# Kernel optimization log

Measured on AMD Instinct MI355X. Metric: run time of the kernel, lower is better.

The kernel has to match this reference:

```python
import jax, jax.numpy as jnp
import numpy as np

B, N, K = 2, 8192, 16          # batch, points, ED_nsample
SA_C, DG_C = 128, 1024         # SA_conv_out, DG_conv_out
CAT_C = SA_C + SA_C // 4 + 4   # 164 channels into head


def _conv1(W, b, x):
    # 1x1 Conv1d: W [out,in], x [B,in,N]
    return jnp.einsum('oc,bcn->bon', W, x) + b[None, :, None]


def _bn_relu(x, g, be):
    # BatchNorm1d (training-mode batch stats) + ReLU, x [B,C,N]
    m = x.mean(axis=(0, 2), keepdims=True)
    v = x.var(axis=(0, 2), keepdims=True)
    return jax.nn.relu((x - m) * jax.lax.rsqrt(v + 1e-5) * g[None, :, None] + be[None, :, None])


def setup_inputs() -> dict:
    key = jax.random.key(0)
    ks = jax.random.split(key, 32)
    w = lambda k, s: jax.random.normal(k, s, jnp.float32) * 0.05
    p = {}
    p['pointcloud'] = jax.random.normal(ks[0], (B, N, 3), jnp.float32)
    p['h1'] = jax.random.normal(ks[1], (B, SA_C, N), jnp.float32)
    p['h2'] = jax.random.normal(ks[2], (B, DG_C, N), jnp.float32)
    p['numpoints'] = N
    # DG head convs 1024->256->64->32
    p['DG_w1'], p['DG_b1'] = w(ks[3], (256, DG_C)), jnp.zeros(256, jnp.float32)
    p['DG_g1'], p['DG_be1'] = jnp.ones(256, jnp.float32), jnp.zeros(256, jnp.float32)
    p['DG_w2'], p['DG_b2'] = w(ks[4], (64, 256)), jnp.zeros(64, jnp.float32)
    p['DG_g2'], p['DG_be2'] = jnp.ones(64, jnp.float32), jnp.zeros(64, jnp.float32)
    p['DG_w3'], p['DG_b3'] = w(ks[5], (SA_C // 4, 64)), jnp.zeros(SA_C // 4, jnp.float32)
    p['DG_g3'], p['DG_be3'] = jnp.ones(SA_C // 4, jnp.float32), jnp.zeros(SA_C // 4, jnp.float32)
    # ED MLP 3->4->4
    p['ED_w1'], p['ED_b1'] = w(ks[6], (3, 4)), jnp.zeros(4, jnp.float32)
    p['ED_w2'], p['ED_b2'] = w(ks[7], (4, 4)), jnp.zeros(4, jnp.float32)
    # head convs 164->512->256->128
    p['C_w1'], p['C_b1'] = w(ks[8], (512, CAT_C)), jnp.zeros(512, jnp.float32)
    p['C_g1'], p['C_be1'] = jnp.ones(512, jnp.float32), jnp.zeros(512, jnp.float32)
    p['C_w2'], p['C_b2'] = w(ks[9], (256, 512)), jnp.zeros(256, jnp.float32)
    p['C_g2'], p['C_be2'] = jnp.ones(256, jnp.float32), jnp.zeros(256, jnp.float32)
    p['C_w3'], p['C_b3'] = w(ks[10], (128, 256)), jnp.zeros(128, jnp.float32)
    p['C_g3'], p['C_be3'] = jnp.ones(128, jnp.float32), jnp.zeros(128, jnp.float32)
    return p


def reference(pointcloud, h1, h2, numpoints,
              DG_w1, DG_b1, DG_g1, DG_be1, DG_w2, DG_b2, DG_g2, DG_be2,
              DG_w3, DG_b3, DG_g3, DG_be3,
              ED_w1, ED_b1, ED_w2, ED_b2,
              C_w1, C_b1, C_g1, C_be1, C_w2, C_b2, C_g2, C_be2,
              C_w3, C_b3, C_g3, C_be3):
    xyz = pointcloud[..., :3]
    # DG branch head
    h2p = _bn_relu(_conv1(DG_w1, DG_b1, h2), DG_g1, DG_be1)
    h2p = _bn_relu(_conv1(DG_w2, DG_b2, h2p), DG_g2, DG_be2)
    h2p = _bn_relu(_conv1(DG_w3, DG_b3, h2p), DG_g3, DG_be3)
    # ED branch: brute-force knn on squared distances
    sq = jnp.sum(xyz * xyz, axis=-1)                               # [B,N]
    d = sq[:, :, None] + sq[:, None, :] - 2.0 * jnp.einsum('bnd,bmd->bnm', xyz, xyz)
    _, idx = jax.lax.top_k(-d, K)                                  # [B,N,K]
    nbr = jax.vmap(lambda pts, i: pts[i])(xyz, idx)                # [B,N,K,3]
    c = nbr - nbr.mean(axis=2, keepdims=True)
    cov = jnp.einsum('bnkd,bnke->bnde', c, c) / K                  # [B,N,3,3]
    ev = jnp.linalg.eigvalsh(cov)                                  # [B,N,3] ascending
    h3 = jax.nn.relu(ev @ ED_w1 + ED_b1) @ ED_w2 + ED_b2           # [B,N,4]
    # fuse and head
    z = jnp.concatenate([h1, h2p, jnp.transpose(h3, (0, 2, 1))], axis=1)
    z = _bn_relu(_conv1(C_w1, C_b1, z), C_g1, C_be1)
    z = _bn_relu(_conv1(C_w2, C_b2, z), C_g2, C_be2)
    z = _bn_relu(_conv1(C_w3, C_b3, z), C_g3, C_be3)
    return xyz, z
```

## Files before the change

### kernel.cpp

```cpp
#include <hip/hip_runtime.h>

#define NPTS 8192
#define BATCH 2

typedef __attribute__((ext_vector_type(8))) __bf16 bf16x8;
typedef __attribute__((ext_vector_type(4))) float f32x4;
typedef unsigned int u32;

__device__ inline unsigned short f2bf(float x) {
    unsigned u = __float_as_uint(x);
    u += 0x7fffu + ((u >> 16) & 1u);
    return (unsigned short)(u >> 16);
}
__device__ inline unsigned pack32(float d, unsigned idx) {
    unsigned u = __float_as_uint(d);
    u ^= ((unsigned)((int)u >> 31)) | 0x80000000u;
    return (u & 0xFFFFE000u) | idx;
}
__device__ inline unsigned bitonic64u(unsigned key, int lane) {
#pragma unroll
    for (int k = 2; k <= 64; k <<= 1) {
#pragma unroll
        for (int j = k >> 1; j > 0; j >>= 1) {
            unsigned o = __shfl_xor(key, j, 64);
            bool tmin = (((lane & k) == 0) == ((lane & j) == 0));
            key = ((o < key) == tmin) ? o : key;
        }
    }
    return key;
}
__device__ inline void ins16(unsigned& key, unsigned c, int lane) {
    unsigned prev = __shfl_up(key, 1, 64);
    if (lane == 0) prev = 0u;
    unsigned mx = prev > c ? prev : c;
    key = mx < key ? mx : key;
}
__device__ inline float distf(float4 q, float4 p) {
    return fmaf(-2.f, fmaf(q.z, p.z, fmaf(q.y, p.y, q.x * p.x)), q.w + p.w);
}

__global__ __launch_bounds__(256) void prep_presplit(
    const float* __restrict__ pc, float* __restrict__ oxyz, float4* __restrict__ pq,
    const float* __restrict__ W0, const float* __restrict__ W1,
    const float* __restrict__ W2, const float* __restrict__ W3,
    const float* __restrict__ W4, const float* __restrict__ W5,
    unsigned short* __restrict__ wsp) {
    int bx = blockIdx.x, tid = threadIdx.x;
    if (bx < 64) {
        int t = bx * 256 + tid;
        float x = pc[t * 3 + 0], y = pc[t * 3 + 1], z = pc[t * 3 + 2];
        oxyz[t * 3 + 0] = x; oxyz[t * 3 + 1] = y; oxyz[t * 3 + 2] = z;
        pq[t] = make_float4(x, y, z, fmaf(z, z, fmaf(y, y, x * x)));
        return;
    }
    int pb = bx - 64;
    const float* W; int O, C, OP; size_t off; int base;
    if (pb < 1024)      { W = W0; O = 256; C = 1024; OP = 256; off = 0;       base = 0; }
    else if (pb < 1152) { W = W1; O =  64; C =  256; OP = 128; off = 524288;  base = 1024; }
    else if (pb < 1184) { W = W2; O =  32; C =   64; OP = 128; off = 589824;  base = 1152; }
    else if (pb < 1568) { W = W3; O = 512; C =  164; OP = 512; off = 606208;  base = 1184; }
    else if (pb < 2080) { W = W4; O = 256; C =  512; OP = 256; off = 802816;  base = 1568; }
    else                { W = W5; O = 128; C =  256; OP = 128; off = 1064960; base = 2080; }
    unsigned short* dst = wsp + off;
    int t = (pb - base) * 256 + tid;
    int kk = t & 31;
    int o = (t >> 5) % OP;
    int kt = t / (OP * 32);
    int c = kt * 32 + kk;
    float x = (o < O && c < C) ? W[o * C + c] : 0.f;
    unsigned short hb = f2bf(x);
    float hf = __uint_as_float((unsigned)hb << 16);
    unsigned short lb = f2bf(x - hf);
    int s = kk >> 3, pos = kk & 7;
    int sst = s ^ ((o >> 1) & 3);
    dst[((size_t)(kt * 2) * OP + o) * 32 + sst * 8 + pos] = hb;
    dst[((size_t)(kt * 2 + 1) * OP + o) * 32 + sst * 8 + pos] = lb;
}

template <int MODE>
__global__ __launch_bounds__(256, 4) void mfma_gemm(
    const unsigned short* __restrict__ Wsp, const float* __restrict__ bias,
    const float* __restrict__ X, float* __restrict__ out,
    int O, int C, int OP, int nK,
    const float2* __restrict__ stats,
    const float* __restrict__ h1, const float* __restrict__ h3,
    const float2* __restrict__ stats3,
    float2* __restrict__ partout) {
    const int N = NPTS;
    int tid = threadIdx.x;
    int lane = tid & 63, w = tid >> 6;
    int wm = w >> 1, wn = w & 1;
    int b = blockIdx.z, n0 = blockIdx.x * 64, o0 = blockIdx.y * 64;
    int nblk = blockIdx.x;
    int n = n0 + lane;

    __shared__ __align__(16) unsigned char lds[18432];
    __shared__ float ps1[2][64], ps2[2][64];
    unsigned char* WHp = lds;
    unsigned char* WLp = lds + 4096;
    unsigned char* XHp = lds + 8192;
    unsigned char* XLp = lds + 13312;

    f32x4 acc[2][2];
#pragma unroll
    for (int i = 0; i < 2; ++i)
#pragma unroll
        for (int j = 0; j < 2; ++j) acc[i][j] = (f32x4){0.f, 0.f, 0.f, 0.f};

    float xcur[8], xnxt[8];
    auto loadx = [&](int kt, float (&dst)[8]) {
#pragma unroll
        for (int i = 0; i < 8; ++i) {
            int c = kt * 32 + w * 8 + i;
            float x = 0.f;
            if (MODE == 0 || MODE == 1) {
                if (c < C) x = X[((size_t)(b * C + c)) * N + n];
            } else {
                if (c < 128)       x = h1[((size_t)(b * 128 + c)) * N + n];
                else if (c < 160)  x = X[((size_t)(b * 32 + (c - 128))) * N + n];
                else if (c < 164)  x = h3[((size_t)(b * 4 + (c - 160))) * N + n];
            }
            dst[i] = x;
        }
    };

    loadx(0, xcur);
    for (int kt = 0; kt < nK; ++kt) {
        int c0 = kt * 32;
#pragma unroll
        for (int comp = 0; comp < 2; ++comp) {
            const unsigned short* gb = Wsp + ((size_t)(kt * 2 + comp) * OP + o0) * 32;
            unsigned char* lb = comp ? WLp : WHp;
            __builtin_amdgcn_global_load_lds(
                (const __attribute__((address_space(1))) u32*)(gb + w * 512 + lane * 8),
                (__attribute__((address_space(3))) u32*)(lb + w * 1024),
                16, 0, 0);
        }
        {
            union { bf16x8 s; unsigned short u[8]; } hh, ll;
#pragma unroll
            for (int i = 0; i < 8; ++i) {
                int c = c0 + w * 8 + i;
                float x = xcur[i];
                if (MODE == 1) {
                    if (c < C) {
                        float2 st = stats[c];
                        x = fmaxf(fmaf(x, st.x, st.y), 0.f);
                    }
                } else if (MODE == 2) {
                    if (c >= 128 && c < 160) {
                        float2 st = stats3[c - 128];
                        x = fmaxf(fmaf(x, st.x, st.y), 0.f);
                    }
                }
                unsigned short hb = f2bf(x);
                float hf = __uint_as_float((unsigned)hb << 16);
                unsigned short lb = f2bf(x - hf);
                hh.u[i] = hb; ll.u[i] = lb;
            }
            *(bf16x8*)(XHp + lane * 80 + w * 16) = hh.s;
            *(bf16x8*)(XLp + lane * 80 + w * 16) = ll.s;
        }
        if (kt + 1 < nK) loadx(kt + 1, xnxt);
        __syncthreads();
        {
            int koff = (lane >> 4) * 16;
            bf16x8 bh[2], bl[2];
#pragma unroll
            for (int ni = 0; ni < 2; ++ni) {
                int rb = wn * 32 + ni * 16 + (lane & 15);
                bh[ni] = *(const bf16x8*)(XHp + rb * 80 + koff);
                bl[ni] = *(const bf16x8*)(XLp + rb * 80 + koff);
            }
#pragma unroll
            for (int mi = 0; mi < 2; ++mi) {
                int ra = wm * 32 + mi * 16 + (lane & 15);
                int sw = koff ^ ((((unsigned)ra >> 1) & 3) * 16);
                bf16x8 ah = *(const bf16x8*)(WHp + ra * 64 + sw);
                bf16x8 al = *(const bf16x8*)(WLp + ra * 64 + sw);
#pragma unroll
                for (int ni = 0; ni < 2; ++ni) {
                    acc[mi][ni] = __builtin_amdgcn_mfma_f32_16x16x32_bf16(ah, bh[ni], acc[mi][ni], 0, 0, 0);
                    acc[mi][ni] = __builtin_amdgcn_mfma_f32_16x16x32_bf16(ah, bl[ni], acc[mi][ni], 0, 0, 0);
                    acc[mi][ni] = __builtin_amdgcn_mfma_f32_16x16x32_bf16(al, bh[ni], acc[mi][ni], 0, 0, 0);
                }
            }
        }
        __syncthreads();
        if (kt + 1 < nK) {
#pragma unroll
            for (int i = 0; i < 8; ++i) xcur[i] = xnxt[i];
        }
    }
    int col = lane & 15, rq = lane >> 4;
#pragma unroll
    for (int mi = 0; mi < 2; ++mi) {
#pragma unroll
        for (int j = 0; j < 4; ++j) {
            int oloc = wm * 32 + mi * 16 + rq * 4 + j;
            int o = o0 + oloc;
            float s1 = 0.f, s2 = 0.f;
            if (o < O) {
                float bs = bias[o];
                float v0 = acc[mi][0][j] + bs;
                float v1 = acc[mi][1][j] + bs;
                float* po = out + ((size_t)(b * O + o)) * N + n0 + wn * 32 + col;
                po[0] = v0; po[16] = v1;
                s1 = v0 + v1;
                s2 = fmaf(v0, v0, v1 * v1);
            }
#pragma unroll
            for (int mm = 1; mm < 16; mm <<= 1) {
                s1 += __shfl_xor(s1, mm, 64);
                s2 += __shfl_xor(s2, mm, 64);
            }
            if (col == 0) { ps1[wn][oloc] = s1; ps2[wn][oloc] = s2; }
        }
    }
    __syncthreads();
    if (tid < 64) {
        int o = o0 + tid;
        if (o < O)
            partout[(size_t)o * 256 + b * 128 + nblk] =
                make_float2(ps1[0][tid] + ps1[1][tid], ps2[0][tid] + ps2[1][tid]);
    }
}

__global__ __launch_bounds__(256) void finalize_kernel(const float2* __restrict__ part,
                                                       const float* __restrict__ g,
                                                       const float* __restrict__ be,
                                                       float2* __restrict__ st) {
    int c = blockIdx.x;
    int tid = threadIdx.x;
    __shared__ float r1[256], r2[256];
    float2 v = part[(size_t)c * 256 + tid];
    r1[tid] = v.x; r2[tid] = v.y;
    __syncthreads();
    for (int off = 128; off > 0; off >>= 1) {
        if (tid < off) { r1[tid] += r1[tid + off]; r2[tid] += r2[tid + off]; }
        __syncthreads();
    }
    if (tid == 0) {
        const float inv = 1.f / (BATCH * NPTS);
        float m = r1[0] * inv;
        float var = r2[0] * inv - m * m;
        float sc = g[c] * rsqrtf(var + 1e-5f);
        st[c] = make_float2(sc, be[c] - m * sc);
    }
}

__global__ __launch_bounds__(256) void stats_final_kernel(
    const float2* __restrict__ part, const float* __restrict__ g,
    const float* __restrict__ be, const float* __restrict__ X,
    float* __restrict__ outz) {
    const int N = NPTS;
    const int C = 128;
    int c = blockIdx.x;
    int tid = threadIdx.x;
    __shared__ float r1[256], r2[256];
    __shared__ float2 stv;
    float2 v = part[(size_t)c * 256 + tid];
    r1[tid] = v.x; r2[tid] = v.y;
    __syncthreads();
    for (int off = 128; off > 0; off >>= 1) {
        if (tid < off) { r1[tid] += r1[tid + off]; r2[tid] += r2[tid + off]; }
        __syncthreads();
    }
    if (tid == 0) {
        const float inv = 1.f / (BATCH * NPTS);
        float m = r1[0] * inv;
        float var = r2[0] * inv - m * m;
        float sc = g[c] * rsqrtf(var + 1e-5f);
        stv = make_float2(sc, be[c] - m * sc);
    }
    __syncthreads();
    float2 s = stv;
    for (int b = 0; b < BATCH; ++b) {
        const float* p = X + (size_t)(b * C + c) * N;
        float* q = outz + (size_t)(b * C + c) * N;
        for (int nn = tid * 4; nn < N; nn += 1024) {
            float4 v4 = *(const float4*)(p + nn);
            v4.x = fmaxf(fmaf(v4.x, s.x, s.y), 0.f);
            v4.y = fmaxf(fmaf(v4.y, s.x, s.y), 0.f);
            v4.z = fmaxf(fmaf(v4.z, s.x, s.y), 0.f);
            v4.w = fmaxf(fmaf(v4.w, s.x, s.y), 0.f);
            *(float4*)(q + nn) = v4;
        }
    }
}

__global__ __launch_bounds__(256) void knn_eig_kernel(
    const float4* __restrict__ pq,
    const float* __restrict__ ew1, const float* __restrict__ eb1,
    const float* __restrict__ ew2, const float* __restrict__ eb2,
    float* __restrict__ h3) {
    int wv = threadIdx.x >> 6;
    int lane = threadIdx.x & 63;
    int sg = blockIdx.x * 4 + wv;
    int b = sg >> 12;
    int iloc = (sg & 4095) << 1;
    const float4* pqb = pq + (size_t)b * NPTS;
    float4 Q0 = pqb[iloc + 0], Q1 = pqb[iloc + 1];

    float4 p = pqb[lane];
    unsigned k0 = bitonic64u(pack32(distf(Q0, p), lane), lane);
    unsigned k1 = bitonic64u(pack32(distf(Q1, p), lane), lane);
    unsigned tk0 = (unsigned)__builtin_amdgcn_readlane((int)k0, 15);
    unsigned tk1 = (unsigned)__builtin_amdgcn_readlane((int)k1, 15);

    float4 A = pqb[64 + lane];
    float4 B = pqb[128 + lane];
    for (int it = 1; it + 1 < 128; it += 2) {
        int tbA = it * 64, tbB = tbA + 64;
        int t3 = (it + 3 < 128) ? it + 3 : 0;
        float4 Cx = pqb[(it + 2) * 64 + lane];
        float4 Dx = pqb[t3 * 64 + lane];
        unsigned cA0 = pack32(distf(Q0, A), tbA + lane);
        unsigned cA1 = pack32(distf(Q1, A), tbA + lane);
        unsigned cB0 = pack32(distf(Q0, B), tbB + lane);
        unsigned cB1 = pack32(distf(Q1, B), tbB + lane);
        unsigned long long mA0 = __ballot(cA0 < tk0), mB0 = __ballot(cB0 < tk0);
        unsigned long long mA1 = __ballot(cA1 < tk1), mB1 = __ballot(cB1 < tk1);
        if (mA0 | mA1 | mB0 | mB1) {
            while (mA0) {
                int L = __ffsll((long long)mA0) - 1; mA0 &= mA0 - 1;
                ins16(k0, (unsigned)__builtin_amdgcn_readlane((int)cA0, L), lane);
            }
            while (mB0) {
                int L = __ffsll((long long)mB0) - 1; mB0 &= mB0 - 1;
                ins16(k0, (unsigned)__builtin_amdgcn_readlane((int)cB0, L), lane);
            }
            while (mA1) {
                int L = __ffsll((long long)mA1) - 1; mA1 &= mA1 - 1;
                ins16(k1, (unsigned)__builtin_amdgcn_readlane((int)cA1, L), lane);
            }
            while (mB1) {
                int L = __ffsll((long long)mB1) - 1; mB1 &= mB1 - 1;
                ins16(k1, (unsigned)__builtin_amdgcn_readlane((int)cB1, L), lane);
            }
            tk0 = (unsigned)__builtin_amdgcn_readlane((int)k0, 15);
            tk1 = (unsigned)__builtin_amdgcn_readlane((int)k1, 15);
        }
        A = Cx; B = Dx;
    }
    {
        int tbA = 127 * 64;
        unsigned cA0 = pack32(distf(Q0, A), tbA + lane);
        unsigned cA1 = pack32(distf(Q1, A), tbA + lane);
        unsigned long long mA0 = __ballot(cA0 < tk0);
        unsigned long long mA1 = __ballot(cA1 < tk1);
        while (mA0) {
            int L = __ffsll((long long)mA0) - 1; mA0 &= mA0 - 1;
            ins16(k0, (unsigned)__builtin_amdgcn_readlane((int)cA0, L), lane);
        }
        while (mA1) {
            int L = __ffsll((long long)mA1) - 1; mA1 &= mA1 - 1;
            ins16(k1, (unsigned)__builtin_amdgcn_readlane((int)cA1, L), lane);
        }
    }

    int g = lane >> 4, r = lane & 15;
    unsigned j0 = ((unsigned)__shfl((int)k0, r, 64)) & 8191u;
    unsigned j1 = ((unsigned)__shfl((int)k1, r, 64)) & 8191u;
    unsigned nj = ((g & 1) == 0) ? j0 : j1;

    float4 nb = pqb[nj];
    float sx = nb.x, sy = nb.y, sz = nb.z;
#pragma unroll
    for (int m = 1; m < 16; m <<= 1) {
        sx += __shfl_xor(sx, m, 64);
        sy += __shfl_xor(sy, m, 64);
        sz += __shfl_xor(sz, m, 64);
    }
    const float i16 = 1.f / 16.f;
    float cx = nb.x - sx * i16, cy = nb.y - sy * i16, cz = nb.z - sz * i16;
    float xx = cx * cx, xy = cx * cy, xz = cx * cz, yy = cy * cy, yz = cy * cz, zz = cz * cz;
#pragma unroll
    for (int m = 1; m < 16; m <<= 1) {
        xx += __shfl_xor(xx, m, 64); xy += __shfl_xor(xy, m, 64); xz += __shfl_xor(xz, m, 64);
        yy += __shfl_xor(yy, m, 64); yz += __shfl_xor(yz, m, 64); zz += __shfl_xor(zz, m, 64);
    }
    float a11 = xx * i16, a12 = xy * i16, a13 = xz * i16,
          a22 = yy * i16, a23 = yz * i16, a33 = zz * i16;
    float q = (a11 + a22 + a33) * (1.f / 3.f);
    float p1 = a12 * a12 + a13 * a13 + a23 * a23;
    float b11 = a11 - q, b22 = a22 - q, b33 = a33 - q;
    float p2 = b11 * b11 + b22 * b22 + b33 * b33 + 2.f * p1;
    float pr = sqrtf(p2 * (1.f / 6.f));
    float ipv = (p2 > 1e-32f) ? (1.f / pr) : 0.f;
    float detB = b11 * (b22 * b33 - a23 * a23) - a12 * (a12 * b33 - a23 * a13) +
                 a13 * (a12 * a23 - b22 * a13);
    float r3 = 0.5f * detB * ipv * ipv * ipv;
    r3 = fminf(1.f, fmaxf(-1.f, r3));
    float phi = acosf(r3) * (1.f / 3.f);
    float e1 = q + 2.f * pr * cosf(phi);
    float e3 = q + 2.f * pr * cosf(phi + 2.0943951023931953f);
    float e2 = 3.f * q - e1 - e3;
    float ev0 = e3, ev1 = e2, ev2 = e1;
    float h[4], o[4];
#pragma unroll
    for (int kk = 0; kk < 4; ++kk)
        h[kk] = fmaxf(eb1[kk] + ev0 * ew1[kk] + ev1 * ew1[4 + kk] + ev2 * ew1[8 + kk], 0.f);
#pragma unroll
    for (int kk = 0; kk < 4; ++kk)
        o[kk] = eb2[kk] + h[0] * ew2[kk] + h[1] * ew2[4 + kk] + h[2] * ew2[8 + kk] +
                h[3] * ew2[12 + kk];
    int ipt = iloc + (g & 1);
    if (r == 0 && g < 2) {
#pragma unroll
        for (int kk = 0; kk < 4; ++kk) h3[(b * 4 + kk) * NPTS + ipt] = o[kk];
    }
}

extern "C" void kernel_launch(void* const* d_in, const int* in_sizes, int n_in,
                              void* d_out, int out_size, void* d_ws, size_t ws_size,
                              hipStream_t stream) {
    const float* pc    = (const float*)d_in[0];
    const float* h1    = (const float*)d_in[1];
    const float* h2    = (const float*)d_in[2];
    const float* DG_w1 = (const float*)d_in[4];
    const float* DG_b1 = (const float*)d_in[5];
    const float* DG_g1 = (const float*)d_in[6];
    const float* DG_be1= (const float*)d_in[7];
    const float* DG_w2 = (const float*)d_in[8];
    const float* DG_b2 = (const float*)d_in[9];
    const float* DG_g2 = (const float*)d_in[10];
    const float* DG_be2= (const float*)d_in[11];
    const float* DG_w3 = (const float*)d_in[12];
    const float* DG_b3 = (const float*)d_in[13];
    const float* DG_g3 = (const float*)d_in[14];
    const float* DG_be3= (const float*)d_in[15];
    const float* ED_w1 = (const float*)d_in[16];
    const float* ED_b1 = (const float*)d_in[17];
    const float* ED_w2 = (const float*)d_in[18];
    const float* ED_b2 = (const float*)d_in[19];
    const float* C_w1  = (const float*)d_in[20];
    const float* C_b1  = (const float*)d_in[21];
    const float* C_g1  = (const float*)d_in[22];
    const float* C_be1 = (const float*)d_in[23];
    const float* C_w2  = (const float*)d_in[24];
    const float* C_b2  = (const float*)d_in[25];
    const float* C_g2  = (const float*)d_in[26];
    const float* C_be2 = (const float*)d_in[27];
    const float* C_w3  = (const float*)d_in[28];
    const float* C_b3  = (const float*)d_in[29];
    const float* C_g3  = (const float*)d_in[30];
    const float* C_be3 = (const float*)d_in[31];

    float* ws = (float*)d_ws;
    float* A  = ws;
    float* Bb = ws + (8l << 20);
    float* Cc = ws + (12l << 20);
    float* H3 = ws + (14l << 20);
    float4* PQ = (float4*)(H3 + 65536);
    float2* ST = (float2*)(H3 + 131072);
    unsigned short* WSP = (unsigned short*)(H3 + 131072 + 2560);

    float2* P_DG1 = (float2*)(Bb + (1l << 20));
    float2* P_DG2 = (float2*)(Bb + (1l << 20) + 131072);
    float2* P_DG3 = (float2*)(Bb + (1l << 20) + 131072 + 32768);
    float2* P_C1  = (float2*)(Cc + (1l << 20));
    float2* TAIL  = (float2*)(WSP + 1130496);
    float2* P_C2  = TAIL;
    float2* P_C3  = TAIL + 65536;

    const size_t W1SP = 0;
    const size_t W2SP = 524288;
    const size_t W3SP = 589824;
    const size_t C1SP = 606208;
    const size_t C2SP = 802816;
    const size_t C3SP = 1064960;

    float* outxyz = (float*)d_out;
    float* outz   = (float*)d_out + BATCH * NPTS * 3;

    prep_presplit<<<2272, 256, 0, stream>>>(pc, outxyz, PQ,
                                            DG_w1, DG_w2, DG_w3, C_w1, C_w2, C_w3, WSP);

    mfma_gemm<0><<<dim3(128, 4, 2), 256, 0, stream>>>(WSP + W1SP, DG_b1, h2, A, 256, 1024, 256, 32,
                                                      nullptr, nullptr, nullptr, nullptr, P_DG1);
    finalize_kernel<<<256, 256, 0, stream>>>(P_DG1, DG_g1, DG_be1, ST + 0);
    mfma_gemm<1><<<dim3(128, 1, 2), 256, 0, stream>>>(WSP + W2SP, DG_b2, A, Bb, 64, 256, 128, 8,
                                                      ST + 0, nullptr, nullptr, nullptr, P_DG2);
    finalize_kernel<<<64, 256, 0, stream>>>(P_DG2, DG_g2, DG_be2, ST + 256);
    mfma_gemm<1><<<dim3(128, 1, 2), 256, 0, stream>>>(WSP + W3SP, DG_b3, Bb, Cc, 32, 64, 128, 2,
                                                      ST + 256, nullptr, nullptr, nullptr, P_DG3);
    finalize_kernel<<<32, 256, 0, stream>>>(P_DG3, DG_g3, DG_be3, ST + 320);

    knn_eig_kernel<<<2048, 256, 0, stream>>>(PQ, ED_w1, ED_b1, ED_w2, ED_b2, H3);

    mfma_gemm<2><<<dim3(128, 8, 2), 256, 0, stream>>>(WSP + C1SP, C_b1, Cc, A, 512, 164, 512, 6,
                                                      nullptr, h1, H3, ST + 320, P_C1);
    finalize_kernel<<<512, 256, 0, stream>>>(P_C1, C_g1, C_be1, ST + 352);
    mfma_gemm<1><<<dim3(128, 4, 2), 256, 0, stream>>>(WSP + C2SP, C_b2, A, Bb, 256, 512, 256, 16,
                                                      ST + 352, nullptr, nullptr, nullptr, P_C2);
    finalize_kernel<<<256, 256, 0, stream>>>(P_C2, C_g2, C_be2, ST + 864);
    mfma_gemm<1><<<dim3(128, 2, 2), 256, 0, stream>>>(WSP + C3SP, C_b3, Bb, Cc, 128, 256, 128, 8,
                                                      ST + 864, nullptr, nullptr, nullptr, P_C3);

    stats_final_kernel<<<128, 256, 0, stream>>>(P_C3, C_g3, C_be3, Cc, outz);
}
```

Measured before the change: 276.9 us.

## Fuse first DG GEMM and kNN eigen kernel into one heterogeneous launch

```diff
diff --git a/kernel.cpp b/kernel.cpp
--- a/kernel.cpp
+++ b/kernel.cpp
@@ -78,7 +78,8 @@
 }
 
 template <int MODE>
-__global__ __launch_bounds__(256, 4) void mfma_gemm(
+__device__ __forceinline__ void gemm_body(
+    int nblk, int oy, int b,
     const unsigned short* __restrict__ Wsp, const float* __restrict__ bias,
     const float* __restrict__ X, float* __restrict__ out,
     int O, int C, int OP, int nK,
@@ -90,8 +91,7 @@
     int tid = threadIdx.x;
     int lane = tid & 63, w = tid >> 6;
     int wm = w >> 1, wn = w & 1;
-    int b = blockIdx.z, n0 = blockIdx.x * 64, o0 = blockIdx.y * 64;
-    int nblk = blockIdx.x;
+    int n0 = nblk * 64, o0 = oy * 64;
     int n = n0 + lane;
 
     __shared__ __align__(16) unsigned char lds[18432];
@@ -226,77 +226,26 @@
     }
 }
 
-__global__ __launch_bounds__(256) void finalize_kernel(const float2* __restrict__ part,
-                                                       const float* __restrict__ g,
-                                                       const float* __restrict__ be,
-                                                       float2* __restrict__ st) {
-    int c = blockIdx.x;
-    int tid = threadIdx.x;
-    __shared__ float r1[256], r2[256];
-    float2 v = part[(size_t)c * 256 + tid];
-    r1[tid] = v.x; r2[tid] = v.y;
-    __syncthreads();
-    for (int off = 128; off > 0; off >>= 1) {
-        if (tid < off) { r1[tid] += r1[tid + off]; r2[tid] += r2[tid + off]; }
-        __syncthreads();
-    }
-    if (tid == 0) {
-        const float inv = 1.f / (BATCH * NPTS);
-        float m = r1[0] * inv;
-        float var = r2[0] * inv - m * m;
-        float sc = g[c] * rsqrtf(var + 1e-5f);
-        st[c] = make_float2(sc, be[c] - m * sc);
-    }
-}
-
-__global__ __launch_bounds__(256) void stats_final_kernel(
-    const float2* __restrict__ part, const float* __restrict__ g,
-    const float* __restrict__ be, const float* __restrict__ X,
-    float* __restrict__ outz) {
-    const int N = NPTS;
-    const int C = 128;
-    int c = blockIdx.x;
-    int tid = threadIdx.x;
-    __shared__ float r1[256], r2[256];
-    __shared__ float2 stv;
-    float2 v = part[(size_t)c * 256 + tid];
-    r1[tid] = v.x; r2[tid] = v.y;
-    __syncthreads();
-    for (int off = 128; off > 0; off >>= 1) {
-        if (tid < off) { r1[tid] += r1[tid + off]; r2[tid] += r2[tid + off]; }
-        __syncthreads();
-    }
-    if (tid == 0) {
-        const float inv = 1.f / (BATCH * NPTS);
-        float m = r1[0] * inv;
-        float var = r2[0] * inv - m * m;
-        float sc = g[c] * rsqrtf(var + 1e-5f);
-        stv = make_float2(sc, be[c] - m * sc);
-    }
-    __syncthreads();
-    float2 s = stv;
-    for (int b = 0; b < BATCH; ++b) {
-        const float* p = X + (size_t)(b * C + c) * N;
-        float* q = outz + (size_t)(b * C + c) * N;
-        for (int nn = tid * 4; nn < N; nn += 1024) {
-            float4 v4 = *(const float4*)(p + nn);
-            v4.x = fmaxf(fmaf(v4.x, s.x, s.y), 0.f);
-            v4.y = fmaxf(fmaf(v4.y, s.x, s.y), 0.f);
-            v4.z = fmaxf(fmaf(v4.z, s.x, s.y), 0.f);
-            v4.w = fmaxf(fmaf(v4.w, s.x, s.y), 0.f);
-            *(float4*)(q + nn) = v4;
-        }
-    }
-}
-
-__global__ __launch_bounds__(256) void knn_eig_kernel(
-    const float4* __restrict__ pq,
-    const float* __restrict__ ew1, const float* __restrict__ eb1,
-    const float* __restrict__ ew2, const float* __restrict__ eb2,
-    float* __restrict__ h3) {
+template <int MODE>
+__global__ __launch_bounds__(256, 4) void mfma_gemm(
+    const unsigned short* __restrict__ Wsp, const float* __restrict__ bias,
+    const float* __restrict__ X, float* __restrict__ out,
+    int O, int C, int OP, int nK,
+    const float2* __restrict__ stats,
+    const float* __restrict__ h1, const float* __restrict__ h3,
+    const float2* __restrict__ stats3,
+    float2* __restrict__ partout) {
+    gemm_body<MODE>(blockIdx.x, blockIdx.y, blockIdx.z, Wsp, bias, X, out, O, C, OP, nK,
+                    stats, h1, h3, stats3, partout);
+}
+
+__device__ void knn_body(int kb, const float4* __restrict__ pq,
+                         const float* __restrict__ ew1, const float* __restrict__ eb1,
+                         const float* __restrict__ ew2, const float* __restrict__ eb2,
+                         float* __restrict__ h3) {
     int wv = threadIdx.x >> 6;
     int lane = threadIdx.x & 63;
-    int sg = blockIdx.x * 4 + wv;
+    int sg = kb * 4 + wv;
     int b = sg >> 12;
     int iloc = (sg & 4095) << 1;
     const float4* pqb = pq + (size_t)b * NPTS;
@@ -409,6 +358,85 @@
     if (r == 0 && g < 2) {
 #pragma unroll
         for (int kk = 0; kk < 4; ++kk) h3[(b * 4 + kk) * NPTS + ipt] = o[kk];
+    }
+}
+
+__global__ __launch_bounds__(256, 4) void dg1_knn(
+    const unsigned short* __restrict__ Wsp, const float* __restrict__ bias,
+    const float* __restrict__ X, float* __restrict__ out, float2* __restrict__ partout,
+    const float4* __restrict__ pq,
+    const float* __restrict__ ew1, const float* __restrict__ eb1,
+    const float* __restrict__ ew2, const float* __restrict__ eb2,
+    float* __restrict__ h3) {
+    if (blockIdx.x < 1024) {
+        int bid = blockIdx.x;
+        gemm_body<0>(bid & 127, (bid >> 7) & 3, bid >> 9, Wsp, bias, X, out,
+                     256, 1024, 256, 32, nullptr, nullptr, nullptr, nullptr, partout);
+    } else {
+        knn_body(blockIdx.x - 1024, pq, ew1, eb1, ew2, eb2, h3);
+    }
+}
+
+__global__ __launch_bounds__(256) void finalize_kernel(const float2* __restrict__ part,
+                                                       const float* __restrict__ g,
+                                                       const float* __restrict__ be,
+                                                       float2* __restrict__ st) {
+    int c = blockIdx.x;
+    int tid = threadIdx.x;
+    __shared__ float r1[256], r2[256];
+    float2 v = part[(size_t)c * 256 + tid];
+    r1[tid] = v.x; r2[tid] = v.y;
+    __syncthreads();
+    for (int off = 128; off > 0; off >>= 1) {
+        if (tid < off) { r1[tid] += r1[tid + off]; r2[tid] += r2[tid + off]; }
+        __syncthreads();
+    }
+    if (tid == 0) {
+        const float inv = 1.f / (BATCH * NPTS);
+        float m = r1[0] * inv;
+        float var = r2[0] * inv - m * m;
+        float sc = g[c] * rsqrtf(var + 1e-5f);
+        st[c] = make_float2(sc, be[c] - m * sc);
+    }
+}
+
+__global__ __launch_bounds__(256) void stats_final_kernel(
+    const float2* __restrict__ part, const float* __restrict__ g,
+    const float* __restrict__ be, const float* __restrict__ X,
+    float* __restrict__ outz) {
+    const int N = NPTS;
+    const int C = 128;
+    int c = blockIdx.x;
+    int tid = threadIdx.x;
+    __shared__ float r1[256], r2[256];
+    __shared__ float2 stv;
+    float2 v = part[(size_t)c * 256 + tid];
+    r1[tid] = v.x; r2[tid] = v.y;
+    __syncthreads();
+    for (int off = 128; off > 0; off >>= 1) {
+        if (tid < off) { r1[tid] += r1[tid + off]; r2[tid] += r2[tid + off]; }
+        __syncthreads();
+    }
+    if (tid == 0) {
+        const float inv = 1.f / (BATCH * NPTS);
+        float m = r1[0] * inv;
+        float var = r2[0] * inv - m * m;
+        float sc = g[c] * rsqrtf(var + 1e-5f);
+        stv = make_float2(sc, be[c] - m * sc);
+    }
+    __syncthreads();
+    float2 s = stv;
+    for (int b = 0; b < BATCH; ++b) {
+        const float* p = X + (size_t)(b * C + c) * N;
+        float* q = outz + (size_t)(b * C + c) * N;
+        for (int nn = tid * 4; nn < N; nn += 1024) {
+            float4 v4 = *(const float4*)(p + nn);
+            v4.x = fmaxf(fmaf(v4.x, s.x, s.y), 0.f);
+            v4.y = fmaxf(fmaf(v4.y, s.x, s.y), 0.f);
+            v4.z = fmaxf(fmaf(v4.z, s.x, s.y), 0.f);
+            v4.w = fmaxf(fmaf(v4.w, s.x, s.y), 0.f);
+            *(float4*)(q + nn) = v4;
+        }
     }
 }
 
@@ -477,8 +505,8 @@
     prep_presplit<<<2272, 256, 0, stream>>>(pc, outxyz, PQ,
                                             DG_w1, DG_w2, DG_w3, C_w1, C_w2, C_w3, WSP);
 
-    mfma_gemm<0><<<dim3(128, 4, 2), 256, 0, stream>>>(WSP + W1SP, DG_b1, h2, A, 256, 1024, 256, 32,
-                                                      nullptr, nullptr, nullptr, nullptr, P_DG1);
+    dg1_knn<<<3072, 256, 0, stream>>>(WSP + W1SP, DG_b1, h2, A, P_DG1,
+                                      PQ, ED_w1, ED_b1, ED_w2, ED_b2, H3);
     finalize_kernel<<<256, 256, 0, stream>>>(P_DG1, DG_g1, DG_be1, ST + 0);
     mfma_gemm<1><<<dim3(128, 1, 2), 256, 0, stream>>>(WSP + W2SP, DG_b2, A, Bb, 64, 256, 128, 8,
                                                       ST + 0, nullptr, nullptr, nullptr, P_DG2);
@@ -486,8 +514,6 @@
     mfma_gemm<1><<<dim3(128, 1, 2), 256, 0, stream>>>(WSP + W3SP, DG_b3, Bb, Cc, 32, 64, 128, 2,
                                                       ST + 256, nullptr, nullptr, nullptr, P_DG3);
     finalize_kernel<<<32, 256, 0, stream>>>(P_DG3, DG_g3, DG_be3, ST + 320);
-
-    knn_eig_kernel<<<2048, 256, 0, stream>>>(PQ, ED_w1, ED_b1, ED_w2, ED_b2, H3);
 
     mfma_gemm<2><<<dim3(128, 8, 2), 256, 0, stream>>>(WSP + C1SP, C_b1, Cc, A, 512, 164, 512, 6,
                                                       nullptr, h1, H3, ST + 320, P_C1);
```

New measurement: 263.3 us. -4.9%, faster.
